# Kernel tuning notes

Hardware: AMD Instinct MI355X
Metric: run time of the kernel (lower is better)

Reference implementation:

```python
import jax, jax.numpy as jnp
import numpy as np

B, S, D, H = 8, 1024, 512, 8
DK = D // H
NEG = -1e30  # stands in for -inf; masked probs are zero-filled afterwards, so math matches


def setup_inputs() -> dict:
    rng = jax.random.key(0)
    ks = jax.random.split(rng, 12)
    f = lambda k, shape: jax.random.normal(k, shape, dtype=jnp.float32)
    w = lambda k: f(k, (D, D)) * 0.02  # stored as (in, out); y = x @ W + b
    return {
        "query": f(ks[0], (B, S, D)),
        "key": f(ks[1], (B, S, D)),
        "value": f(ks[2], (B, S, D)),
        "mask": jax.random.randint(ks[3], (B, 1, S), 0, 2, dtype=jnp.int32),
        "Wq": w(ks[4]), "bq": jnp.zeros((D,), jnp.float32),
        "Wk": w(ks[5]), "bk": jnp.zeros((D,), jnp.float32),
        "Wv": w(ks[6]), "bv": jnp.zeros((D,), jnp.float32),
        "Wo": w(ks[7]), "bo": jnp.zeros((D,), jnp.float32),
    }


def reference(query, key, value, mask, Wq, bq, Wk, bk, Wv, bv, Wo, bo):
    # QKV projections -> (B, H, S, DK)
    def proj(x, W, b):
        return (x @ W + b).reshape(B, -1, H, DK).transpose(0, 2, 1, 3)

    q = proj(query, Wq, bq)
    k = proj(key, Wk, bk)
    v = proj(value, Wv, bv)

    scores = jnp.einsum("bhqd,bhkd->bhqk", q, k) / jnp.sqrt(jnp.float32(DK))
    m = (mask[:, None, :, :] == 0)  # (B, 1, 1, S): True where masked out
    scores = jnp.where(m, NEG, scores)
    attn = jax.nn.softmax(scores, axis=-1)
    attn = jnp.where(m, 0.0, attn)  # dropout rate is 0.0 -> identity

    x = jnp.einsum("bhqk,bhkd->bhqd", attn, v)
    x = x.transpose(0, 2, 1, 3).reshape(B, -1, D)  # (B, S, D)
    return x @ Wo + bo
```

## Files before the change

### kernel.cpp

```cpp
#include <hip/hip_runtime.h>
#include <hip/hip_bf16.h>

#define NB 8
#define NS 1024
#define ND 512
#define NH 8
#define NDK 64

typedef __attribute__((ext_vector_type(8))) short bf16x8;
typedef __attribute__((ext_vector_type(4))) float f32x4;
typedef __attribute__((ext_vector_type(16))) float f32x16;

#define QSCALE 0.18033688011112042f
#define NEGBIG -3.0e38f

#define CVTPK(dst, a, b) \
    asm("v_cvt_pk_bf16_f32 %0, %1, %2" : "=v"(dst) : "v"(a), "v"(b))
#define PLSWAP(a, b) \
    asm("v_permlane32_swap_b32 %0, %1" : "+v"(a), "+v"(b))

__device__ __forceinline__ unsigned short bfround(float f) {
    union { float f; unsigned u; } v; v.f = f;
    unsigned u = v.u;
    u += 0x7fffu + ((u >> 16) & 1u);
    return (unsigned short)(u >> 16);
}

__device__ __forceinline__ size_t qf_off(int s, int dk) {
    return ((size_t)(((s >> 5) * 4 + (dk >> 4)) * 64 + ((dk >> 3) & 1) * 32 + (s & 31)) << 3) + (dk & 7);
}
__device__ __forceinline__ size_t kf_off(int s, int dk) {
    return ((size_t)(((s >> 6) * 8 + ((s >> 5) & 1) * 4 + (dk >> 4)) * 64 + ((dk >> 3) & 1) * 32 + (s & 31)) << 3) + (dk & 7);
}
__device__ __forceinline__ size_t vf_off(int s, int dk) {
    return ((size_t)(((s >> 6) * 8 + (dk >> 5) * 4 + ((s >> 4) & 3)) * 64 + ((s >> 3) & 1) * 32 + (dk & 31)) << 3) + (s & 7);
}

__global__ __launch_bounds__(256) void wt_kernel(const float* __restrict__ W0,
                                                 const float* __restrict__ W1,
                                                 const float* __restrict__ W2,
                                                 const float* __restrict__ W3,
                                                 unsigned short* __restrict__ wt) {
    __shared__ float sh[64][65];
    const int z = blockIdx.z;
    const float* W = z == 0 ? W0 : z == 1 ? W1 : z == 2 ? W2 : W3;
    unsigned short* out = wt + (size_t)z * ND * ND;
    const int o0 = blockIdx.x * 64, i0 = blockIdx.y * 64;
    const int tx = threadIdx.x & 63;
    const int ty = threadIdx.x >> 6;
    #pragma unroll
    for (int rr = 0; rr < 16; ++rr) {
        const int row = ty * 16 + rr;
        sh[row][tx] = W[(size_t)(i0 + row) * ND + o0 + tx];
    }
    __syncthreads();
    #pragma unroll
    for (int rr = 0; rr < 16; ++rr) {
        const int row = ty * 16 + rr;
        out[(size_t)(o0 + row) * ND + i0 + tx] = bfround(sh[tx][row]);
    }
}

__global__ __launch_bounds__(256) void gemm_qkv(
    const float* __restrict__ A0, const float* __restrict__ A1, const float* __restrict__ A2,
    const unsigned short* __restrict__ wt,
    const float* __restrict__ b0, const float* __restrict__ b1, const float* __restrict__ b2,
    unsigned short* __restrict__ outb) {
    __shared__ unsigned short Als[2][128 * 40];
    __shared__ unsigned short Bls[2][128 * 40];
    const int t = threadIdx.x;
    const int lane = t & 63, w = t >> 6;
    const int wr = w >> 1, wc = w & 1;
    const int lr = lane & 15, lg = lane >> 4;
    const int bid = blockIdx.x;
    const int u = (bid & 7) * 96 + (bid >> 3);
    const int xt = u & 3, yt = (u >> 2) & 63, z = u >> 8;
    const float* A = z == 0 ? A0 : z == 1 ? A1 : A2;
    const float* bias = z == 0 ? b0 : z == 1 ? b1 : b2;
    const unsigned short* Wt = wt + (size_t)z * ND * ND;
    unsigned short* outp = outb + (size_t)z * NB * NH * NS * NDK;
    const int m0 = yt * 128, n0 = xt * 128;

    const int a_row = w * 32 + (lane >> 3);
    const int a_col = (lane & 7) * 4;
    const int b_row = w * 32 + (lane >> 2);
    const int b_col = (lane & 3) * 8;

    f32x4 acc[4][4];
    #pragma unroll
    for (int i = 0; i < 4; ++i)
        #pragma unroll
        for (int j = 0; j < 4; ++j) acc[i][j] = (f32x4){0.f, 0.f, 0.f, 0.f};

    f32x4 ra[4];
    bf16x8 rbv[2];

#define QKV_LOAD(kt) do {                                                      \
        const int _k0 = (kt) * 32;                                             \
        ra[0] = *(const f32x4*)(A + (size_t)(m0 + a_row + 0)  * ND + _k0 + a_col); \
        ra[1] = *(const f32x4*)(A + (size_t)(m0 + a_row + 8)  * ND + _k0 + a_col); \
        ra[2] = *(const f32x4*)(A + (size_t)(m0 + a_row + 16) * ND + _k0 + a_col); \
        ra[3] = *(const f32x4*)(A + (size_t)(m0 + a_row + 24) * ND + _k0 + a_col); \
        rbv[0] = *(const bf16x8*)(Wt + (size_t)(n0 + b_row + 0)  * ND + _k0 + b_col); \
        rbv[1] = *(const bf16x8*)(Wt + (size_t)(n0 + b_row + 16) * ND + _k0 + b_col); \
    } while (0)

#define QKV_WRITE(p) do {                                                      \
        _Pragma("unroll")                                                      \
        for (int j = 0; j < 4; ++j) {                                          \
            unsigned c0, c1;                                                   \
            CVTPK(c0, ra[j][0], ra[j][1]);                                     \
            CVTPK(c1, ra[j][2], ra[j][3]);                                     \
            uint2 pv; pv.x = c0; pv.y = c1;                                    \
            *(uint2*)(&Als[p][(a_row + j * 8) * 40 + a_col]) = pv;             \
        }                                                                      \
        _Pragma("unroll")                                                      \
        for (int j = 0; j < 2; ++j) {                                          \
            union { bf16x8 v; uint2 h[2]; } ub; ub.v = rbv[j];                 \
            *(uint2*)(&Bls[p][(b_row + j * 16) * 40 + b_col]) = ub.h[0];       \
            *(uint2*)(&Bls[p][(b_row + j * 16) * 40 + b_col + 4]) = ub.h[1];   \
        }                                                                      \
    } while (0)

#define QKV_COMPUTE(p) do {                                                    \
        bf16x8 af[4], bfr[4];                                                  \
        _Pragma("unroll")                                                      \
        for (int mi = 0; mi < 4; ++mi)                                         \
            af[mi] = *(const bf16x8*)(&Als[p][(wr * 64 + mi * 16 + lr) * 40 + lg * 8]); \
        _Pragma("unroll")                                                      \
        for (int nj = 0; nj < 4; ++nj)                                         \
            bfr[nj] = *(const bf16x8*)(&Bls[p][(wc * 64 + nj * 16 + lr) * 40 + lg * 8]); \
        __builtin_amdgcn_s_setprio(1);                                         \
        _Pragma("unroll")                                                      \
        for (int mi = 0; mi < 4; ++mi)                                         \
            _Pragma("unroll")                                                  \
            for (int nj = 0; nj < 4; ++nj)                                     \
                acc[mi][nj] = __builtin_amdgcn_mfma_f32_16x16x32_bf16(         \
                    af[mi], bfr[nj], acc[mi][nj], 0, 0, 0);                    \
        __builtin_amdgcn_s_setprio(0);                                         \
    } while (0)

    QKV_LOAD(0);
    QKV_WRITE(0);
    QKV_LOAD(1);
    __syncthreads();
    #pragma unroll 1
    for (int kt = 0; kt < 15; ++kt) {
        QKV_COMPUTE(kt & 1);
        QKV_WRITE((kt + 1) & 1);
        if (kt < 14) QKV_LOAD(kt + 2);
        __syncthreads();
    }
    QKV_COMPUTE(1);
#undef QKV_LOAD
#undef QKV_WRITE
#undef QKV_COMPUTE

    const float osc = z == 0 ? QSCALE : 1.0f;
    #pragma unroll
    for (int mi = 0; mi < 4; ++mi) {
        #pragma unroll
        for (int nj = 0; nj < 4; ++nj) {
            const int n = n0 + wc * 64 + nj * 16 + lr;
            const float bv = bias[n];
            #pragma unroll
            for (int r = 0; r < 4; ++r) {
                const int m = m0 + wr * 64 + mi * 16 + lg * 4 + r;
                const float val = (acc[mi][nj][r] + bv) * osc;
                const int bb = m >> 10, s = m & 1023;
                const int hh = n >> 6, dk = n & 63;
                const size_t off = z == 0 ? qf_off(s, dk)
                                 : z == 1 ? kf_off(s, dk)
                                          : vf_off(s, dk);
                outp[((size_t)(bb * NH + hh) << 16) + off] = bfround(val);
            }
        }
    }
}

__global__ __launch_bounds__(256) void gemm_out(
    const unsigned short* __restrict__ Xb, const unsigned short* __restrict__ Wt,
    const float* __restrict__ bo, float* __restrict__ outp) {
    __shared__ unsigned short Ao[2][128 * 40];
    __shared__ unsigned short Bo[2][64 * 40];
    const int t = threadIdx.x;
    const int lane = t & 63, w = t >> 6;
    const int wr = w >> 1, wc = w & 1;
    const int lr = lane & 15, lg = lane >> 4;
    const int bid = blockIdx.x;
    const int u = (bid & 7) * 64 + (bid >> 3);
    const int xt = u & 7, yt = u >> 3;
    const int m0 = yt * 128, n0 = xt * 64;

    const int a_row = w * 32 + (lane >> 2);
    const int b_row = w * 16 + (lane >> 2);
    const int gc = (lane & 3) * 8;

    f32x4 acc[4][2];
    #pragma unroll
    for (int i = 0; i < 4; ++i)
        #pragma unroll
        for (int j = 0; j < 2; ++j) acc[i][j] = (f32x4){0.f, 0.f, 0.f, 0.f};

    bf16x8 raa[2], rbb;

#define OUT_LOAD(kt) do {                                                      \
        const int _k0 = (kt) * 32;                                             \
        raa[0] = *(const bf16x8*)(Xb + (size_t)(m0 + a_row + 0)  * ND + _k0 + gc); \
        raa[1] = *(const bf16x8*)(Xb + (size_t)(m0 + a_row + 16) * ND + _k0 + gc); \
        rbb    = *(const bf16x8*)(Wt + (size_t)(n0 + b_row) * ND + _k0 + gc);  \
    } while (0)

#define OUT_WRITE(p) do {                                                      \
        _Pragma("unroll")                                                      \
        for (int j = 0; j < 2; ++j) {                                          \
            union { bf16x8 v; uint2 h[2]; } ua; ua.v = raa[j];                 \
            *(uint2*)(&Ao[p][(a_row + j * 16) * 40 + gc]) = ua.h[0];           \
            *(uint2*)(&Ao[p][(a_row + j * 16) * 40 + gc + 4]) = ua.h[1];       \
        }                                                                      \
        {                                                                      \
            union { bf16x8 v; uint2 h[2]; } ub; ub.v = rbb;                    \
            *(uint2*)(&Bo[p][b_row * 40 + gc]) = ub.h[0];                      \
            *(uint2*)(&Bo[p][b_row * 40 + gc + 4]) = ub.h[1];                  \
        }                                                                      \
    } while (0)

#define OUT_COMPUTE(p) do {                                                    \
        bf16x8 af[4], bfr[2];                                                  \
        _Pragma("unroll")                                                      \
        for (int mi = 0; mi < 4; ++mi)                                         \
            af[mi] = *(const bf16x8*)(&Ao[p][(wr * 64 + mi * 16 + lr) * 40 + lg * 8]); \
        _Pragma("unroll")                                                      \
        for (int nj = 0; nj < 2; ++nj)                                         \
            bfr[nj] = *(const bf16x8*)(&Bo[p][(wc * 32 + nj * 16 + lr) * 40 + lg * 8]); \
        __builtin_amdgcn_s_setprio(1);                                         \
        _Pragma("unroll")                                                      \
        for (int mi = 0; mi < 4; ++mi)                                         \
            _Pragma("unroll")                                                  \
            for (int nj = 0; nj < 2; ++nj)                                     \
                acc[mi][nj] = __builtin_amdgcn_mfma_f32_16x16x32_bf16(         \
                    af[mi], bfr[nj], acc[mi][nj], 0, 0, 0);                    \
        __builtin_amdgcn_s_setprio(0);                                         \
    } while (0)

    OUT_LOAD(0);
    OUT_WRITE(0);
    OUT_LOAD(1);
    __syncthreads();
    #pragma unroll 1
    for (int kt = 0; kt < 15; ++kt) {
        OUT_COMPUTE(kt & 1);
        OUT_WRITE((kt + 1) & 1);
        if (kt < 14) OUT_LOAD(kt + 2);
        __syncthreads();
    }
    OUT_COMPUTE(1);
#undef OUT_LOAD
#undef OUT_WRITE
#undef OUT_COMPUTE

    #pragma unroll
    for (int mi = 0; mi < 4; ++mi) {
        #pragma unroll
        for (int nj = 0; nj < 2; ++nj) {
            const int n = n0 + wc * 32 + nj * 16 + lr;
            const float bv = bo[n];
            #pragma unroll
            for (int r = 0; r < 4; ++r) {
                const int m = m0 + wr * 64 + mi * 16 + lg * 4 + r;
                outp[(size_t)m * ND + n] = acc[mi][nj][r] + bv;
            }
        }
    }
}

struct AttnState {
    f32x16 acc0, acc1;
    float m_st, l_st;
};

__device__ __forceinline__ void attn_step(const bf16x8 (&kf)[8], const bf16x8 (&vv)[8],
                                          const bf16x8 (&qf)[4], int mval,
                                          float* __restrict__ brow, int lane, int hi,
                                          AttnState& st) {
    brow[lane] = mval ? 0.f : NEGBIG;

    f32x16 sc0 = {}, sc1 = {};
    __builtin_amdgcn_s_setprio(1);
    sc0 = __builtin_amdgcn_mfma_f32_32x32x16_bf16(kf[0], qf[0], sc0, 0, 0, 0);
    sc1 = __builtin_amdgcn_mfma_f32_32x32x16_bf16(kf[4], qf[0], sc1, 0, 0, 0);
    sc0 = __builtin_amdgcn_mfma_f32_32x32x16_bf16(kf[1], qf[1], sc0, 0, 0, 0);
    sc1 = __builtin_amdgcn_mfma_f32_32x32x16_bf16(kf[5], qf[1], sc1, 0, 0, 0);
    sc0 = __builtin_amdgcn_mfma_f32_32x32x16_bf16(kf[2], qf[2], sc0, 0, 0, 0);
    sc1 = __builtin_amdgcn_mfma_f32_32x32x16_bf16(kf[6], qf[2], sc1, 0, 0, 0);
    sc0 = __builtin_amdgcn_mfma_f32_32x32x16_bf16(kf[3], qf[3], sc0, 0, 0, 0);
    sc1 = __builtin_amdgcn_mfma_f32_32x32x16_bf16(kf[7], qf[3], sc1, 0, 0, 0);
    __builtin_amdgcn_s_setprio(0);

    {
        const float* bl = brow + 4 * hi;
        #pragma unroll
        for (int mm = 0; mm < 4; ++mm) {
            const f32x4 bv0 = *(const f32x4*)(bl + 8 * mm);
            const f32x4 bv1 = *(const f32x4*)(bl + 32 + 8 * mm);
            #pragma unroll
            for (int c = 0; c < 4; ++c) {
                sc0[4 * mm + c] += bv0[c];
                sc1[4 * mm + c] += bv1[c];
            }
        }
    }

    float tv[16];
    #pragma unroll
    for (int r = 0; r < 16; ++r) tv[r] = fmaxf(sc0[r], sc1[r]);
    #pragma unroll
    for (int s = 8; s > 0; s >>= 1)
        #pragma unroll
        for (int r = 0; r < 16; ++r)
            if (r < s) tv[r] = fmaxf(tv[r], tv[r + s]);
    const float mx = fmaxf(tv[0], __shfl_xor(tv[0], 32));
    const float mn = fmaxf(st.m_st, mx);

    #pragma unroll
    for (int r = 0; r < 16; ++r) {
        sc0[r] = __builtin_amdgcn_exp2f(sc0[r] - mn);
        sc1[r] = __builtin_amdgcn_exp2f(sc1[r] - mn);
    }
    #pragma unroll
    for (int r = 0; r < 16; ++r) tv[r] = sc0[r] + sc1[r];
    #pragma unroll
    for (int s = 8; s > 0; s >>= 1)
        #pragma unroll
        for (int r = 0; r < 16; ++r)
            if (r < s) tv[r] += tv[r + s];
    const float rs = tv[0] + __shfl_xor(tv[0], 32);

    const bool ch = mn > st.m_st;
    if (__any(ch)) {
        const float f = __builtin_amdgcn_exp2f(st.m_st - mn);
        st.l_st = st.l_st * f + rs;
        st.m_st = mn;
        #pragma unroll
        for (int r = 0; r < 16; ++r) { st.acc0[r] *= f; st.acc1[r] *= f; }
    } else {
        st.l_st += rs;
    }

    union U8 { unsigned u[4]; bf16x8 v; };
    bf16x8 pA0, pA1, pB0, pB1;
    {
        unsigned w00, w01, w10, w11, w20, w21, w30, w31;
        CVTPK(w00, sc0[0], sc0[1]);  CVTPK(w01, sc0[2], sc0[3]);
        CVTPK(w10, sc0[4], sc0[5]);  CVTPK(w11, sc0[6], sc0[7]);
        CVTPK(w20, sc0[8], sc0[9]);  CVTPK(w21, sc0[10], sc0[11]);
        CVTPK(w30, sc0[12], sc0[13]); CVTPK(w31, sc0[14], sc0[15]);
        PLSWAP(w00, w10); PLSWAP(w01, w11);
        PLSWAP(w20, w30); PLSWAP(w21, w31);
        U8 f0; f0.u[0] = w00; f0.u[1] = w01; f0.u[2] = w10; f0.u[3] = w11;
        U8 f1; f1.u[0] = w20; f1.u[1] = w21; f1.u[2] = w30; f1.u[3] = w31;
        pA0 = f0.v; pA1 = f1.v;
    }
    {
        unsigned w00, w01, w10, w11, w20, w21, w30, w31;
        CVTPK(w00, sc1[0], sc1[1]);  CVTPK(w01, sc1[2], sc1[3]);
        CVTPK(w10, sc1[4], sc1[5]);  CVTPK(w11, sc1[6], sc1[7]);
        CVTPK(w20, sc1[8], sc1[9]);  CVTPK(w21, sc1[10], sc1[11]);
        CVTPK(w30, sc1[12], sc1[13]); CVTPK(w31, sc1[14], sc1[15]);
        PLSWAP(w00, w10); PLSWAP(w01, w11);
        PLSWAP(w20, w30); PLSWAP(w21, w31);
        U8 f0; f0.u[0] = w00; f0.u[1] = w01; f0.u[2] = w10; f0.u[3] = w11;
        U8 f1; f1.u[0] = w20; f1.u[1] = w21; f1.u[2] = w30; f1.u[3] = w31;
        pB0 = f0.v; pB1 = f1.v;
    }

    __builtin_amdgcn_s_setprio(1);
    st.acc0 = __builtin_amdgcn_mfma_f32_32x32x16_bf16(vv[0], pA0, st.acc0, 0, 0, 0);
    st.acc1 = __builtin_amdgcn_mfma_f32_32x32x16_bf16(vv[4], pA0, st.acc1, 0, 0, 0);
    st.acc0 = __builtin_amdgcn_mfma_f32_32x32x16_bf16(vv[1], pA1, st.acc0, 0, 0, 0);
    st.acc1 = __builtin_amdgcn_mfma_f32_32x32x16_bf16(vv[5], pA1, st.acc1, 0, 0, 0);
    st.acc0 = __builtin_amdgcn_mfma_f32_32x32x16_bf16(vv[2], pB0, st.acc0, 0, 0, 0);
    st.acc1 = __builtin_amdgcn_mfma_f32_32x32x16_bf16(vv[6], pB0, st.acc1, 0, 0, 0);
    st.acc0 = __builtin_amdgcn_mfma_f32_32x32x16_bf16(vv[3], pB1, st.acc0, 0, 0, 0);
    st.acc1 = __builtin_amdgcn_mfma_f32_32x32x16_bf16(vv[7], pB1, st.acc1, 0, 0, 0);
    __builtin_amdgcn_s_setprio(0);
}

__global__ __launch_bounds__(256, 2) void attn_kernel(const unsigned short* __restrict__ QF,
                                                      const unsigned short* __restrict__ KF,
                                                      const unsigned short* __restrict__ VF,
                                                      const int* __restrict__ mask,
                                                      unsigned short* __restrict__ Xb) {
    __shared__ float bias_lds[4][64];
    const int t = threadIdx.x;
    const int lane = t & 63, w = t >> 6;
    const int q32 = lane & 31, hi = lane >> 5;
    const int bid = blockIdx.x;
    const int u = (bid & 7) * 64 + (bid >> 3);
    const int bh = u >> 3, xq = u & 7;
    const int b = bh >> 3, h = bh & 7;
    const int q = xq * 128 + w * 32 + q32;
    const unsigned short* QFh = QF + ((size_t)bh << 16);
    const unsigned short* KFh = KF + ((size_t)bh << 16);
    const unsigned short* VFh = VF + ((size_t)bh << 16);
    const int* mk = mask + b * NS;
    float* brow = &bias_lds[w][0];

    bf16x8 qf[4];
    {
        const unsigned short* Qp = QFh + (size_t)(xq * 16 + w * 4) * 512 + lane * 8;
        qf[0] = *(const bf16x8*)(Qp + 0 * 512);
        qf[1] = *(const bf16x8*)(Qp + 1 * 512);
        qf[2] = *(const bf16x8*)(Qp + 2 * 512);
        qf[3] = *(const bf16x8*)(Qp + 3 * 512);
    }

    AttnState st;
    st.acc0 = (f32x16){}; st.acc1 = (f32x16){};
    st.m_st = -1.0e30f; st.l_st = 0.f;

    bf16x8 kA[8], kB[8], vv[8];

#define LOADK(dst, itx) do {                                                   \
        const unsigned short* _p = KFh + (size_t)(itx) * 4096 + lane * 8;      \
        dst[0] = *(const bf16x8*)(_p + 0 * 512);                               \
        dst[1] = *(const bf16x8*)(_p + 1 * 512);                               \
        dst[2] = *(const bf16x8*)(_p + 2 * 512);                               \
        dst[3] = *(const bf16x8*)(_p + 3 * 512);                               \
        dst[4] = *(const bf16x8*)(_p + 4 * 512);                               \
        dst[5] = *(const bf16x8*)(_p + 5 * 512);                               \
        dst[6] = *(const bf16x8*)(_p + 6 * 512);                               \
        dst[7] = *(const bf16x8*)(_p + 7 * 512);                               \
    } while (0)

#define LOADV(dst, itx) do {                                                   \
        const unsigned short* _p = VFh + (size_t)(itx) * 4096 + lane * 8;      \
        dst[0] = *(const bf16x8*)(_p + 0 * 512);                               \
        dst[1] = *(const bf16x8*)(_p + 1 * 512);                               \
        dst[2] = *(const bf16x8*)(_p + 2 * 512);                               \
        dst[3] = *(const bf16x8*)(_p + 3 * 512);                               \
        dst[4] = *(const bf16x8*)(_p + 4 * 512);                               \
        dst[5] = *(const bf16x8*)(_p + 5 * 512);                               \
        dst[6] = *(const bf16x8*)(_p + 6 * 512);                               \
        dst[7] = *(const bf16x8*)(_p + 7 * 512);                               \
    } while (0)

    LOADK(kA, 0);
    #pragma unroll 1
    for (int ii = 0; ii < 8; ++ii) {
        const int itE = ii * 2, itO = itE + 1;
        const int mE = mk[itE * 64 + lane];
        LOADV(vv, itE);
        LOADK(kB, itO);
        __builtin_amdgcn_sched_barrier(0);
        attn_step(kA, vv, qf, mE, brow, lane, hi, st);
        const int mO = mk[itO * 64 + lane];
        const int itN = itO + 1 > 15 ? 15 : itO + 1;
        LOADV(vv, itO);
        LOADK(kA, itN);
        __builtin_amdgcn_sched_barrier(0);
        attn_step(kB, vv, qf, mO, brow, lane, hi, st);
    }
#undef LOADK
#undef LOADV

    const float inv = st.l_st > 0.f ? 1.f / st.l_st : 0.f;
    unsigned short* Xp = Xb + (size_t)(b * NS + q) * ND + h * 64 + 4 * hi;
    #pragma unroll
    for (int mm = 0; mm < 4; ++mm) {
        unsigned w0, w1;
        CVTPK(w0, st.acc0[4 * mm] * inv, st.acc0[4 * mm + 1] * inv);
        CVTPK(w1, st.acc0[4 * mm + 2] * inv, st.acc0[4 * mm + 3] * inv);
        uint2 pv; pv.x = w0; pv.y = w1;
        *(uint2*)(Xp + 8 * mm) = pv;
        CVTPK(w0, st.acc1[4 * mm] * inv, st.acc1[4 * mm + 1] * inv);
        CVTPK(w1, st.acc1[4 * mm + 2] * inv, st.acc1[4 * mm + 3] * inv);
        pv.x = w0; pv.y = w1;
        *(uint2*)(Xp + 32 + 8 * mm) = pv;
    }
}

extern "C" void kernel_launch(void* const* d_in, const int* in_sizes, int n_in,
                              void* d_out, int out_size, void* d_ws, size_t ws_size,
                              hipStream_t stream) {
    const float* query = (const float*)d_in[0];
    const float* key   = (const float*)d_in[1];
    const float* value = (const float*)d_in[2];
    const int*   mask  = (const int*)d_in[3];
    const float* Wq = (const float*)d_in[4];
    const float* bq = (const float*)d_in[5];
    const float* Wk = (const float*)d_in[6];
    const float* bk = (const float*)d_in[7];
    const float* Wv = (const float*)d_in[8];
    const float* bv = (const float*)d_in[9];
    const float* Wo = (const float*)d_in[10];
    const float* bo = (const float*)d_in[11];

    const size_t HEADSZ = (size_t)NB * NH * NS * NDK;
    unsigned short* wt = (unsigned short*)d_ws;
    unsigned short* QFb = wt + (size_t)4 * ND * ND;
    unsigned short* KFb = QFb + HEADSZ;
    unsigned short* VFb = KFb + HEADSZ;
    unsigned short* Xb  = VFb + HEADSZ;

    wt_kernel<<<dim3(8, 8, 4), 256, 0, stream>>>(Wq, Wk, Wv, Wo, wt);

    gemm_qkv<<<768, 256, 0, stream>>>(query, key, value, wt, bq, bk, bv, QFb);

    attn_kernel<<<512, 256, 0, stream>>>(QFb, KFb, VFb, mask, Xb);

    gemm_out<<<512, 256, 0, stream>>>(Xb, wt + (size_t)3 * ND * ND, bo, (float*)d_out);
}
```

Before: 81.99 us.

## Halve GEMM M-tiles and stage QKV epilogue through swizzled LDS for coalesced stores

Both projection GEMMs drop from 128-row to 64-row tiles, doubling grid size (1536 and 1024 blocks) to fill more CUs. gemm_qkv gains a launch-bounds occupancy hint and a single shared buffer. Its epilogue now writes bf16 results into an XOR-swizzled LDS tile and emits 16-byte coalesced stores in the fragment layouts the attention kernel expects, replacing scattered 2-byte stores. LDS fills also become single 16-byte writes. The tradeoff is less reuse per block and an extra barrier plus LDS round trip in the epilogue.

Result: no change. 80.47 us (-1.9%).

```diff
diff --git a/kernel.cpp b/kernel.cpp
--- a/kernel.cpp
+++ b/kernel.cpp
@@ -26,15 +26,6 @@
     return (unsigned short)(u >> 16);
 }
 
-__device__ __forceinline__ size_t qf_off(int s, int dk) {
-    return ((size_t)(((s >> 5) * 4 + (dk >> 4)) * 64 + ((dk >> 3) & 1) * 32 + (s & 31)) << 3) + (dk & 7);
-}
-__device__ __forceinline__ size_t kf_off(int s, int dk) {
-    return ((size_t)(((s >> 6) * 8 + ((s >> 5) & 1) * 4 + (dk >> 4)) * 64 + ((dk >> 3) & 1) * 32 + (s & 31)) << 3) + (dk & 7);
-}
-__device__ __forceinline__ size_t vf_off(int s, int dk) {
-    return ((size_t)(((s >> 6) * 8 + (dk >> 5) * 4 + ((s >> 4) & 3)) * 64 + ((s >> 3) & 1) * 32 + (dk & 31)) << 3) + (s & 7);
-}
 
 __global__ __launch_bounds__(256) void wt_kernel(const float* __restrict__ W0,
                                                  const float* __restrict__ W1,
@@ -61,78 +52,72 @@
     }
 }
 
-__global__ __launch_bounds__(256) void gemm_qkv(
+__global__ __launch_bounds__(256, 5) void gemm_qkv(
     const float* __restrict__ A0, const float* __restrict__ A1, const float* __restrict__ A2,
     const unsigned short* __restrict__ wt,
     const float* __restrict__ b0, const float* __restrict__ b1, const float* __restrict__ b2,
     unsigned short* __restrict__ outb) {
-    __shared__ unsigned short Als[2][128 * 40];
-    __shared__ unsigned short Bls[2][128 * 40];
+    __shared__ unsigned short SM[15360];
     const int t = threadIdx.x;
     const int lane = t & 63, w = t >> 6;
     const int wr = w >> 1, wc = w & 1;
     const int lr = lane & 15, lg = lane >> 4;
     const int bid = blockIdx.x;
-    const int u = (bid & 7) * 96 + (bid >> 3);
-    const int xt = u & 3, yt = (u >> 2) & 63, z = u >> 8;
+    const int u = (bid & 7) * 192 + (bid >> 3);
+    const int xt = u & 3, yt = (u >> 2) & 127, z = u >> 9;
     const float* A = z == 0 ? A0 : z == 1 ? A1 : A2;
     const float* bias = z == 0 ? b0 : z == 1 ? b1 : b2;
     const unsigned short* Wt = wt + (size_t)z * ND * ND;
     unsigned short* outp = outb + (size_t)z * NB * NH * NS * NDK;
-    const int m0 = yt * 128, n0 = xt * 128;
-
-    const int a_row = w * 32 + (lane >> 3);
-    const int a_col = (lane & 7) * 4;
-    const int b_row = w * 32 + (lane >> 2);
-    const int b_col = (lane & 3) * 8;
-
-    f32x4 acc[4][4];
-    #pragma unroll
-    for (int i = 0; i < 4; ++i)
+    const int m0 = yt * 64, n0 = xt * 128;
+
+    const int a_row = t >> 3;
+    const int a_col = (t & 7) * 4;
+    const int b_row = t >> 2;
+    const int b_col = (t & 3) * 8;
+
+    f32x4 acc[2][4];
+    #pragma unroll
+    for (int i = 0; i < 2; ++i)
         #pragma unroll
         for (int j = 0; j < 4; ++j) acc[i][j] = (f32x4){0.f, 0.f, 0.f, 0.f};
 
-    f32x4 ra[4];
+    f32x4 ra[2];
     bf16x8 rbv[2];
 
 #define QKV_LOAD(kt) do {                                                      \
         const int _k0 = (kt) * 32;                                             \
-        ra[0] = *(const f32x4*)(A + (size_t)(m0 + a_row + 0)  * ND + _k0 + a_col); \
-        ra[1] = *(const f32x4*)(A + (size_t)(m0 + a_row + 8)  * ND + _k0 + a_col); \
-        ra[2] = *(const f32x4*)(A + (size_t)(m0 + a_row + 16) * ND + _k0 + a_col); \
-        ra[3] = *(const f32x4*)(A + (size_t)(m0 + a_row + 24) * ND + _k0 + a_col); \
-        rbv[0] = *(const bf16x8*)(Wt + (size_t)(n0 + b_row + 0)  * ND + _k0 + b_col); \
-        rbv[1] = *(const bf16x8*)(Wt + (size_t)(n0 + b_row + 16) * ND + _k0 + b_col); \
+        ra[0] = *(const f32x4*)(A + (size_t)(m0 + a_row) * ND + _k0 + a_col);  \
+        ra[1] = *(const f32x4*)(A + (size_t)(m0 + a_row + 32) * ND + _k0 + a_col); \
+        rbv[0] = *(const bf16x8*)(Wt + (size_t)(n0 + b_row) * ND + _k0 + b_col); \
+        rbv[1] = *(const bf16x8*)(Wt + (size_t)(n0 + b_row + 64) * ND + _k0 + b_col); \
     } while (0)
 
 #define QKV_WRITE(p) do {                                                      \
         _Pragma("unroll")                                                      \
-        for (int j = 0; j < 4; ++j) {                                          \
+        for (int j = 0; j < 2; ++j) {                                          \
             unsigned c0, c1;                                                   \
             CVTPK(c0, ra[j][0], ra[j][1]);                                     \
             CVTPK(c1, ra[j][2], ra[j][3]);                                     \
             uint2 pv; pv.x = c0; pv.y = c1;                                    \
-            *(uint2*)(&Als[p][(a_row + j * 8) * 40 + a_col]) = pv;             \
+            *(uint2*)(&SM[(p) * 2560 + (a_row + j * 32) * 40 + a_col]) = pv;   \
         }                                                                      \
         _Pragma("unroll")                                                      \
-        for (int j = 0; j < 2; ++j) {                                          \
-            union { bf16x8 v; uint2 h[2]; } ub; ub.v = rbv[j];                 \
-            *(uint2*)(&Bls[p][(b_row + j * 16) * 40 + b_col]) = ub.h[0];       \
-            *(uint2*)(&Bls[p][(b_row + j * 16) * 40 + b_col + 4]) = ub.h[1];   \
-        }                                                                      \
+        for (int j = 0; j < 2; ++j)                                            \
+            *(bf16x8*)(&SM[5120 + (p) * 5120 + (b_row + j * 64) * 40 + b_col]) = rbv[j]; \
     } while (0)
 
 #define QKV_COMPUTE(p) do {                                                    \
-        bf16x8 af[4], bfr[4];                                                  \
-        _Pragma("unroll")                                                      \
-        for (int mi = 0; mi < 4; ++mi)                                         \
-            af[mi] = *(const bf16x8*)(&Als[p][(wr * 64 + mi * 16 + lr) * 40 + lg * 8]); \
+        bf16x8 af[2], bfr[4];                                                  \
+        _Pragma("unroll")                                                      \
+        for (int mi = 0; mi < 2; ++mi)                                         \
+            af[mi] = *(const bf16x8*)(&SM[(p) * 2560 + (wr * 32 + mi * 16 + lr) * 40 + lg * 8]); \
         _Pragma("unroll")                                                      \
         for (int nj = 0; nj < 4; ++nj)                                         \
-            bfr[nj] = *(const bf16x8*)(&Bls[p][(wc * 64 + nj * 16 + lr) * 40 + lg * 8]); \
+            bfr[nj] = *(const bf16x8*)(&SM[5120 + (p) * 5120 + (wc * 64 + nj * 16 + lr) * 40 + lg * 8]); \
         __builtin_amdgcn_s_setprio(1);                                         \
         _Pragma("unroll")                                                      \
-        for (int mi = 0; mi < 4; ++mi)                                         \
+        for (int mi = 0; mi < 2; ++mi)                                         \
             _Pragma("unroll")                                                  \
             for (int nj = 0; nj < 4; ++nj)                                     \
                 acc[mi][nj] = __builtin_amdgcn_mfma_f32_16x16x32_bf16(         \
@@ -156,24 +141,67 @@
 #undef QKV_WRITE
 #undef QKV_COMPUTE
 
+    __syncthreads();
     const float osc = z == 0 ? QSCALE : 1.0f;
-    #pragma unroll
-    for (int mi = 0; mi < 4; ++mi) {
-        #pragma unroll
-        for (int nj = 0; nj < 4; ++nj) {
-            const int n = n0 + wc * 64 + nj * 16 + lr;
-            const float bv = bias[n];
+    const int bb = m0 >> 10;
+    char* const C = (char*)SM;
+    if (z <= 1) {
+        #pragma unroll
+        for (int mi = 0; mi < 2; ++mi)
             #pragma unroll
-            for (int r = 0; r < 4; ++r) {
-                const int m = m0 + wr * 64 + mi * 16 + lg * 4 + r;
-                const float val = (acc[mi][nj][r] + bv) * osc;
-                const int bb = m >> 10, s = m & 1023;
-                const int hh = n >> 6, dk = n & 63;
-                const size_t off = z == 0 ? qf_off(s, dk)
-                                 : z == 1 ? kf_off(s, dk)
-                                          : vf_off(s, dk);
-                outp[((size_t)(bb * NH + hh) << 16) + off] = bfround(val);
+            for (int nj = 0; nj < 4; ++nj) {
+                const int coln = wc * 64 + nj * 16 + lr;
+                const float bv = bias[n0 + coln];
+                #pragma unroll
+                for (int r = 0; r < 4; ++r) {
+                    const int row = wr * 32 + mi * 16 + lg * 4 + r;
+                    unsigned off = (unsigned)(row * 256 + coln * 2);
+                    off ^= (row & 7) << 4;
+                    *(unsigned short*)(C + off) = bfround((acc[mi][nj][r] + bv) * osc);
+                }
             }
+        __syncthreads();
+        const unsigned cb = ((unsigned)(m0 & 1023) >> 5) * 4;
+        #pragma unroll
+        for (int cc = 0; cc < 4; ++cc) {
+            const int c = w * 4 + cc;
+            const int sub = c >> 3, hhl = (c >> 2) & 1, kk = c & 3;
+            const int row = sub * 32 + (lane & 31);
+            unsigned off = (unsigned)(row * 256 + (hhl * 64 + kk * 16 + (lane >> 5) * 8) * 2);
+            off ^= (row & 7) << 4;
+            const bf16x8 v8 = *(const bf16x8*)(C + off);
+            const int hh = xt * 2 + hhl;
+            *(bf16x8*)(outp + (((size_t)(bb * NH + hh)) << 16) +
+                       (size_t)(cb + sub * 4 + kk) * 512 + lane * 8) = v8;
+        }
+    } else {
+        #pragma unroll
+        for (int mi = 0; mi < 2; ++mi)
+            #pragma unroll
+            for (int nj = 0; nj < 4; ++nj) {
+                const int dkl = wc * 64 + nj * 16 + lr;
+                const float bv = bias[n0 + dkl];
+                #pragma unroll
+                for (int r = 0; r < 4; ++r) {
+                    const int sl = wr * 32 + mi * 16 + lg * 4 + r;
+                    unsigned off = (unsigned)(dkl * 128 + sl * 2);
+                    off ^= (dkl & 7) << 4;
+                    *(unsigned short*)(C + off) = bfround(acc[mi][nj][r] + bv);
+                }
+            }
+        __syncthreads();
+        const unsigned it8 = ((unsigned)(m0 & 1023) >> 6) * 8;
+        #pragma unroll
+        for (int cc = 0; cc < 4; ++cc) {
+            const int c = w * 4 + cc;
+            const int hhl = c >> 3, od = (c >> 2) & 1, s4 = c & 3;
+            const int row = hhl * 64 + od * 32 + (lane & 31);
+            unsigned off = (unsigned)(row * 128 + (s4 * 16 + (lane >> 5) * 8) * 2);
+            off ^= (row & 7) << 4;
+            const bf16x8 v8 = *(const bf16x8*)(C + off);
+            const int hh = xt * 2 + hhl;
+            *(bf16x8*)(outp + (((size_t)(bb * NH + hh)) << 16) +
+                       (size_t)(it8 + od * 4 + s4) * 512 + lane * 8) = v8;
         }
     }
 }
@@ -181,61 +209,49 @@
 __global__ __launch_bounds__(256) void gemm_out(
     const unsigned short* __restrict__ Xb, const unsigned short* __restrict__ Wt,
     const float* __restrict__ bo, float* __restrict__ outp) {
-    __shared__ unsigned short Ao[2][128 * 40];
-    __shared__ unsigned short Bo[2][64 * 40];
+    __shared__ unsigned short SM2[10240];
     const int t = threadIdx.x;
     const int lane = t & 63, w = t >> 6;
     const int wr = w >> 1, wc = w & 1;
     const int lr = lane & 15, lg = lane >> 4;
     const int bid = blockIdx.x;
-    const int u = (bid & 7) * 64 + (bid >> 3);
+    const int u = (bid & 7) * 128 + (bid >> 3);
     const int xt = u & 7, yt = u >> 3;
-    const int m0 = yt * 128, n0 = xt * 64;
-
-    const int a_row = w * 32 + (lane >> 2);
-    const int b_row = w * 16 + (lane >> 2);
-    const int gc = (lane & 3) * 8;
-
-    f32x4 acc[4][2];
-    #pragma unroll
-    for (int i = 0; i < 4; ++i)
+    const int m0 = yt * 64, n0 = xt * 64;
+
+    const int s_row = t >> 2;
+    const int s_col = (t & 3) * 8;
+
+    f32x4 acc[2][2];
+    #pragma unroll
+    for (int i = 0; i < 2; ++i)
         #pragma unroll
         for (int j = 0; j < 2; ++j) acc[i][j] = (f32x4){0.f, 0.f, 0.f, 0.f};
 
-    bf16x8 raa[2], rbb;
+    bf16x8 raa, rbb;
 
 #define OUT_LOAD(kt) do {                                                      \
         const int _k0 = (kt) * 32;                                             \
-        raa[0] = *(const bf16x8*)(Xb + (size_t)(m0 + a_row + 0)  * ND + _k0 + gc); \
-        raa[1] = *(const bf16x8*)(Xb + (size_t)(m0 + a_row + 16) * ND + _k0 + gc); \
-        rbb    = *(const bf16x8*)(Wt + (size_t)(n0 + b_row) * ND + _k0 + gc);  \
+        raa = *(const bf16x8*)(Xb + (size_t)(m0 + s_row) * ND + _k0 + s_col);  \
+        rbb = *(const bf16x8*)(Wt + (size_t)(n0 + s_row) * ND + _k0 + s_col);  \
     } while (0)
 
 #define OUT_WRITE(p) do {                                                      \
-        _Pragma("unroll")                                                      \
-        for (int j = 0; j < 2; ++j) {                                          \
-            union { bf16x8 v; uint2 h[2]; } ua; ua.v = raa[j];                 \
-            *(uint2*)(&Ao[p][(a_row + j * 16) * 40 + gc]) = ua.h[0];           \
-            *(uint2*)(&Ao[p][(a_row + j * 16) * 40 + gc + 4]) = ua.h[1];       \
-        }                                                                      \
-        {                                                                      \
-            union { bf16x8 v; uint2 h[2]; } ub; ub.v = rbb;                    \
-            *(uint2*)(&Bo[p][b_row * 40 + gc]) = ub.h[0];                      \
-            *(uint2*)(&Bo[p][b_row * 40 + gc + 4]) = ub.h[1];                  \
-        }                                                                      \
+        *(bf16x8*)(&SM2[(p) * 2560 + s_row * 40 + s_col]) = raa;               \
+        *(bf16x8*)(&SM2[5120 + (p) * 2560 + s_row * 40 + s_col]) = rbb;        \
     } while (0)
 
 #define OUT_COMPUTE(p) do {                                                    \
-        bf16x8 af[4], bfr[2];                                                  \
-        _Pragma("unroll")                                                      \
-        for (int mi = 0; mi < 4; ++mi)                                         \
-            af[mi] = *(const bf16x8*)(&Ao[p][(wr * 64 + mi * 16 + lr) * 40 + lg * 8]); \
+        bf16x8 af[2], bfr[2];                                                  \
+        _Pragma("unroll")                                                      \
+        for (int mi = 0; mi < 2; ++mi)                                         \
+            af[mi] = *(const bf16x8*)(&SM2[(p) * 2560 + (wr * 32 + mi * 16 + lr) * 40 + lg * 8]); \
         _Pragma("unroll")                                                      \
         for (int nj = 0; nj < 2; ++nj)                                         \
-            bfr[nj] = *(const bf16x8*)(&Bo[p][(wc * 32 + nj * 16 + lr) * 40 + lg * 8]); \
+            bfr[nj] = *(const bf16x8*)(&SM2[5120 + (p) * 2560 + (wc * 32 + nj * 16 + lr) * 40 + lg * 8]); \
         __builtin_amdgcn_s_setprio(1);                                         \
         _Pragma("unroll")                                                      \
-        for (int mi = 0; mi < 4; ++mi)                                         \
+        for (int mi = 0; mi < 2; ++mi)                                         \
             _Pragma("unroll")                                                  \
             for (int nj = 0; nj < 2; ++nj)                                     \
                 acc[mi][nj] = __builtin_amdgcn_mfma_f32_16x16x32_bf16(         \
@@ -260,14 +276,14 @@
 #undef OUT_COMPUTE
 
     #pragma unroll
-    for (int mi = 0; mi < 4; ++mi) {
+    for (int mi = 0; mi < 2; ++mi) {
         #pragma unroll
         for (int nj = 0; nj < 2; ++nj) {
             const int n = n0 + wc * 32 + nj * 16 + lr;
             const float bv = bo[n];
             #pragma unroll
             for (int r = 0; r < 4; ++r) {
-                const int m = m0 + wr * 64 + mi * 16 + lg * 4 + r;
+                const int m = m0 + wr * 32 + mi * 16 + lg * 4 + r;
                 outp[(size_t)m * ND + n] = acc[mi][nj][r] + bv;
             }
         }
@@ -505,9 +521,9 @@
 
     wt_kernel<<<dim3(8, 8, 4), 256, 0, stream>>>(Wq, Wk, Wv, Wo, wt);
 
-    gemm_qkv<<<768, 256, 0, stream>>>(query, key, value, wt, bq, bk, bv, QFb);
+    gemm_qkv<<<1536, 256, 0, stream>>>(query, key, value, wt, bq, bk, bv, QFb);
 
     attn_kernel<<<512, 256, 0, stream>>>(QFb, KFb, VFb, mask, Xb);
 
-    gemm_out<<<512, 256, 0, stream>>>(Xb, wt + (size_t)3 * ND * ND, bo, (float*)d_out);
-}
+    gemm_out<<<1024, 256, 0, stream>>>(Xb, wt + (size_t)3 * ND * ND, bo, (float*)d_out);
+}
```
